# Kernel tuning notes

Measured on AMD Instinct MI355X. Metric: run time of the kernel, lower is better.

Reference implementation:

```python
import jax, jax.numpy as jnp
import numpy as np

B, L, D_PAIR, N_HEAD = 1, 320, 128, 4
EPS = 1e-5


def setup_inputs() -> dict:
    key = jax.random.key(0)
    ks = jax.random.split(key, 8)
    s = 0.05  # ~xavier scale for fan_in=128
    return {
        "pair": jax.random.normal(ks[0], (B, L, L, D_PAIR), jnp.float32),
        "norm_w": jnp.ones((D_PAIR,), jnp.float32),
        "norm_b": jnp.zeros((D_PAIR,), jnp.float32),
        "Wq": jax.random.normal(ks[1], (D_PAIR, D_PAIR), jnp.float32) * s,
        "Wk": jax.random.normal(ks[2], (D_PAIR, D_PAIR), jnp.float32) * s,
        "Wv": jax.random.normal(ks[3], (D_PAIR, D_PAIR), jnp.float32) * s,
        "Wg": jax.random.normal(ks[4], (D_PAIR, D_PAIR), jnp.float32) * s,
        "bg": jnp.zeros((D_PAIR,), jnp.float32),
        "Wo": jax.random.normal(ks[5], (D_PAIR, D_PAIR), jnp.float32) * s,
        "bo": jnp.zeros((D_PAIR,), jnp.float32),
        "Wb": jax.random.normal(ks[6], (N_HEAD, D_PAIR), jnp.float32) * s,
    }


def reference(pair, norm_w, norm_b, Wq, Wk, Wv, Wg, bg, Wo, bo, Wb):
    # Triangle attention, mode='start' (no permute). pair: (B, L, L, D)
    Bs, Ls, _, D = pair.shape
    H = Wb.shape[0]
    Dh = D // H
    scale = Dh ** -0.5

    # LayerNorm (fp32, matches torch eps=1e-5)
    mu = jnp.mean(pair, axis=-1, keepdims=True)
    var = jnp.var(pair, axis=-1, keepdims=True)
    x = (pair - mu) * jax.lax.rsqrt(var + EPS) * norm_w + norm_b

    def heads(y):
        # (B,L,L,D) -> (B,L,H,L,Dh): attention runs along the second L axis per row i
        return y.reshape(Bs, Ls, Ls, H, Dh).transpose(0, 1, 3, 2, 4)

    Q = heads(x @ Wq.T)
    K = heads(x @ Wk.T)
    V = heads(x @ Wv.T)
    g = heads(jax.nn.sigmoid(x @ Wg.T + bg))

    attn = jnp.einsum('blhid,blhjd->blhij', Q, K) * scale  # (B,L,H,L,L)
    # bias from RAW pair (pre-norm), projected to heads, broadcast over query index i
    bias = (pair @ Wb.T).transpose(0, 1, 3, 2)[:, :, :, None, :]  # (B,L,H,1,L)
    attn = jax.nn.softmax(attn + bias, axis=-1)

    out = jnp.einsum('blhij,blhjd->blhid', attn, V)  # (B,L,H,L,Dh)
    out = (g * out).transpose(0, 1, 3, 2, 4).reshape(Bs, Ls, Ls, D)
    return pair + out @ Wo.T + bo
```

## Files before the change

kernel.cpp:

```cpp
#include <hip/hip_runtime.h>

typedef unsigned short u16;
typedef unsigned int u32;
typedef __attribute__((ext_vector_type(8))) short bf16x8;
typedef __attribute__((ext_vector_type(4))) float f32x4;
typedef __attribute__((ext_vector_type(2))) unsigned int u32x2;

#define LOG2E 1.4426950408889634f

__device__ __forceinline__ u16 f2bf(float f) {
    u32 u = __float_as_uint(f);
    u += 0x7fffu + ((u >> 16) & 1u);
    return (u16)(u >> 16);
}
__device__ __forceinline__ u32 pk_bf_trunc(float hi, float lo) {
    return __builtin_amdgcn_perm(__float_as_uint(hi), __float_as_uint(lo), 0x07060302u);
}

__global__ void wconv_kernel(const float* __restrict__ Wq, const float* __restrict__ Wk,
                             const float* __restrict__ Wv, const float* __restrict__ Wg,
                             const float* __restrict__ Wo, const float* __restrict__ norm_w,
                             const float* __restrict__ norm_b, const float* __restrict__ bg,
                             u16* __restrict__ wbf, float* __restrict__ cvec) {
    int b = blockIdx.x;
    if (b < 64) {
        int idx = b * 256 + threadIdx.x;
        float w = norm_w[idx & 127];
        wbf[0 * 16384 + idx] = f2bf(Wq[idx] * w);
        wbf[1 * 16384 + idx] = f2bf(Wk[idx] * w);
        wbf[2 * 16384 + idx] = f2bf(Wv[idx] * w);
        wbf[3 * 16384 + idx] = f2bf(Wg[idx] * w);
        wbf[4 * 16384 + idx] = f2bf(Wo[idx]);
    } else {
        int m = b - 64;
        int n = threadIdx.x;
        if (n < 128) {
            const float* W = (m == 0) ? Wq : (m == 1) ? Wk : (m == 2) ? Wv : Wg;
            float c = 0.f;
#pragma unroll
            for (int k4 = 0; k4 < 32; ++k4) {
                f32x4 bb = *(const f32x4*)&norm_b[k4 * 4];
                f32x4 ww = *(const f32x4*)&W[n * 128 + k4 * 4];
                c += bb[0] * ww[0] + bb[1] * ww[1] + bb[2] * ww[2] + bb[3] * ww[3];
            }
            if (m == 3) c += bg[n];
            cvec[m * 128 + n] = c;
        }
    }
}

#define KS_OFF 9216
#define VTS_OFF 22016
#define PB_W 1152

__global__ __launch_bounds__(512, 4)
void attn_kernel(const float* __restrict__ pair,
                 const float* __restrict__ Wb,
                 const u16* __restrict__ wbf,
                 const float* __restrict__ cvec,
                 u16* __restrict__ Obf,
                 u16* __restrict__ Gg) {
    const int l = blockIdx.x >> 2;
    const int h = blockIdx.x & 3;
    const int tid = threadIdx.x;
    const int wave = tid >> 6;
    const int lane = tid & 63;
    const int i_lo = lane & 15;
    const int q = lane >> 4;

    __shared__ __align__(16) u16 smem[32576];
    __shared__ __align__(16) float biasLds[320];

    const int row_g = tid >> 3;
    const int c8 = tid & 7;
    const int wrow = (wave & 3) * 16;
    const int nth_flip = wave >> 2;

    f32x4 wbv[4];
#pragma unroll
    for (int u = 0; u < 4; ++u)
        wbv[u] = *(const f32x4*)&Wb[h * 128 + c8 * 16 + u * 4];

    float cQ[2], cK[2], cV[2], cG[2];
#pragma unroll
    for (int half = 0; half < 2; ++half) {
        int n = h * 32 + half * 16 + i_lo;
        cQ[half] = cvec[0 * 128 + n];
        cK[half] = cvec[1 * 128 + n];
        cV[half] = cvec[2 * 128 + n];
        cG[half] = cvec[3 * 128 + n];
    }

    u32 qkeep[3][4];

#pragma unroll 1
    for (int t = 0; t < 5; ++t) {
        const int j0 = t * 64;
        const float* prow = pair + ((size_t)(l * 320 + j0 + row_g)) * 128 + c8 * 16;
        f32x4 pr[4];
#pragma unroll
        for (int u = 0; u < 4; ++u) pr[u] = *(const f32x4*)(prow + u * 4);

        float s = 0.f, s2 = 0.f, bd = 0.f;
#pragma unroll
        for (int u = 0; u < 4; ++u) {
            f32x4 p = pr[u];
            f32x4 wb4 = wbv[u];
            s += p[0] + p[1] + p[2] + p[3];
            s2 += p[0] * p[0] + p[1] * p[1] + p[2] * p[2] + p[3] * p[3];
            bd += p[0] * wb4[0] + p[1] * wb4[1] + p[2] * wb4[2] + p[3] * wb4[3];
        }
        s += __shfl_xor(s, 1);   s += __shfl_xor(s, 2);   s += __shfl_xor(s, 4);
        s2 += __shfl_xor(s2, 1); s2 += __shfl_xor(s2, 2); s2 += __shfl_xor(s2, 4);
        bd += __shfl_xor(bd, 1); bd += __shfl_xor(bd, 2); bd += __shfl_xor(bd, 4);
        float mu = s * 0.0078125f;
        float var = s2 * 0.0078125f - mu * mu;
        float rs = rsqrtf(var + 1e-5f);

        __syncthreads();
#pragma unroll
        for (int u = 0; u < 4; ++u) {
            f32x4 p = pr[u];
            ushort4 xv;
            xv.x = f2bf((p[0] - mu) * rs);
            xv.y = f2bf((p[1] - mu) * rs);
            xv.z = f2bf((p[2] - mu) * rs);
            xv.w = f2bf((p[3] - mu) * rs);
            *(ushort4*)&smem[row_g * 136 + c8 * 16 + u * 4] = xv;
        }
        if (c8 == 0) biasLds[j0 + row_g] = bd * LOG2E;
        __syncthreads();

        const int nth = (t & 1) ^ nth_flip;
        f32x4 acc[4];
#pragma unroll
        for (int n2 = 0; n2 < 4; ++n2) acc[n2] = (f32x4){0.f, 0.f, 0.f, 0.f};
#pragma unroll
        for (int kc = 0; kc < 4; ++kc) {
            bf16x8 a = *(const bf16x8*)&smem[(wrow + i_lo) * 136 + kc * 32 + q * 8];
#pragma unroll
            for (int n2 = 0; n2 < 4; ++n2) {
                int nt = nth * 4 + n2;
                bf16x8 wf = *(const bf16x8*)&wbf[(nt >> 1) * 16384 +
                                                 (h * 32 + (nt & 1) * 16 + i_lo) * 128 + kc * 32 + q * 8];
                acc[n2] = __builtin_amdgcn_mfma_f32_16x16x32_bf16(a, wf, acc[n2], 0, 0, 0);
            }
        }
        const int jrow = j0 + wrow + q * 4;
        if (nth == 0) {
            const int ti = t >> 1;
#pragma unroll
            for (int dd = 0; dd < 2; ++dd)
#pragma unroll
                for (int rr = 0; rr < 2; ++rr)
                    qkeep[ti][dd * 2 + rr] =
                        (u32)f2bf(acc[dd][rr * 2] + cQ[dd]) |
                        ((u32)f2bf(acc[dd][rr * 2 + 1] + cQ[dd]) << 16);
#pragma unroll
            for (int n2 = 2; n2 < 4; ++n2)
#pragma unroll
                for (int r = 0; r < 4; ++r)
                    smem[KS_OFF + (jrow + r) * 40 + (n2 & 1) * 16 + i_lo] =
                        f2bf(acc[n2][r] + cK[n2 & 1]);
        } else {
#pragma unroll
            for (int n2 = 0; n2 < 2; ++n2)
#pragma unroll
                for (int r = 0; r < 4; ++r)
                    smem[VTS_OFF + (n2 * 16 + i_lo) * 330 + jrow + r] =
                        f2bf(acc[n2][r] + cV[n2]);
#pragma unroll
            for (int n2 = 2; n2 < 4; ++n2)
#pragma unroll
                for (int r = 0; r < 4; ++r) {
                    float z = acc[n2][r] + cG[n2 & 1];
                    float g = 1.0f / (1.0f + exp2f(-z * LOG2E));
                    Gg[((size_t)((l * 4 + h) * 320 + jrow + r)) * 32 + (n2 & 1) * 16 + i_lo] = f2bf(g);
                }
        }
    }
    __syncthreads();

    const float SC = 0.17677669529663687f * LOG2E;
    const f32x4 zero4 = {0.f, 0.f, 0.f, 0.f};
    u16* pb = smem + wave * PB_W;
    const int nstrip = (wave < 4) ? 3 : 2;
#pragma unroll 1
    for (int t2 = 0; t2 < nstrip; ++t2) {
        const int i0 = (wave + 8 * t2) * 16;
#pragma unroll
        for (int dd = 0; dd < 2; ++dd)
#pragma unroll
            for (int rr = 0; rr < 2; ++rr) {
                u32 v = qkeep[t2][dd * 2 + rr];
                pb[(q * 4 + rr * 2) * 40 + dd * 16 + i_lo] = (u16)v;
                pb[(q * 4 + rr * 2 + 1) * 40 + dd * 16 + i_lo] = (u16)(v >> 16);
            }
        bf16x8 qf = *(const bf16x8*)&pb[i_lo * 40 + q * 8];

        f32x4 oacc[2];
        oacc[0] = zero4; oacc[1] = zero4;
        float sum = 0.f;
#pragma unroll 1
        for (int c = 0; c < 5; ++c) {
            f32x4 sc4[4];
#pragma unroll
            for (int jt = 0; jt < 4; ++jt) {
                bf16x8 kf = *(const bf16x8*)&smem[KS_OFF + (c * 64 + jt * 16 + i_lo) * 40 + q * 8];
                sc4[jt] = __builtin_amdgcn_mfma_f32_16x16x32_bf16(kf, qf, zero4, 0, 0, 0);
            }
#pragma unroll
            for (int jt = 0; jt < 4; ++jt) {
                f32x4 b4 = *(const f32x4*)&biasLds[c * 64 + jt * 16 + q * 4];
#pragma unroll
                for (int r = 0; r < 4; ++r) {
                    float p = exp2f(sc4[jt][r] * SC + b4[r]);
                    sc4[jt][r] = p;
                    sum += p;
                }
            }
#pragma unroll
            for (int jt = 0; jt < 4; ++jt) {
                u32x2 pk;
                pk.x = pk_bf_trunc(sc4[jt][1], sc4[jt][0]);
                pk.y = pk_bf_trunc(sc4[jt][3], sc4[jt][2]);
                *(u32x2*)&pb[i_lo * 72 + jt * 16 + q * 4] = pk;
            }
#pragma unroll
            for (int kt2 = 0; kt2 < 2; ++kt2) {
                bf16x8 pf = *(const bf16x8*)&pb[i_lo * 72 + kt2 * 32 + q * 8];
#pragma unroll
                for (int mt = 0; mt < 2; ++mt) {
                    bf16x8 vf = *(const bf16x8*)&smem[VTS_OFF + (mt * 16 + i_lo) * 330 +
                                                      c * 64 + kt2 * 32 + q * 8];
                    oacc[mt] = __builtin_amdgcn_mfma_f32_16x16x32_bf16(vf, pf, oacc[mt], 0, 0, 0);
                }
            }
        }
        sum += __shfl_xor(sum, 16);
        sum += __shfl_xor(sum, 32);
        float rinv = 1.0f / sum;
#pragma unroll
        for (int mt = 0; mt < 2; ++mt) {
            u32x2 pk;
            pk.x = pk_bf_trunc(oacc[mt][1] * rinv, oacc[mt][0] * rinv);
            pk.y = pk_bf_trunc(oacc[mt][3] * rinv, oacc[mt][2] * rinv);
            *(u32x2*)&Obf[((size_t)(l * 320 + i0 + i_lo)) * 128 + h * 32 + mt * 16 + q * 4] = pk;
        }
    }
}

__global__ __launch_bounds__(512, 6)
void outproj_kernel(const float* __restrict__ pair,
                    const float* __restrict__ bo,
                    const u16* __restrict__ Obf,
                    const u16* __restrict__ Gg,
                    const u16* __restrict__ wbf,
                    float* __restrict__ out) {
    const int tid = threadIdx.x;
    const int wave = tid >> 6;
    const int lane = tid & 63;
    const int i_lo = lane & 15;
    const int q = lane >> 4;

    __shared__ __align__(16) u16 WoLds[128 * 132];
    const u16* Wo = wbf + 4 * 16384;
#pragma unroll
    for (int it = 0; it < 4; ++it) {
        int unit = it * 512 + tid;
        int n = unit >> 4, k8 = unit & 15;
        *(bf16x8*)&WoLds[n * 132 + k8 * 8] = *(const bf16x8*)&Wo[unit * 8];
    }
    __syncthreads();

    const int row0 = blockIdx.x * 128 + wave * 16;
    const int lidx = row0 / 320;
    const int irow = row0 - lidx * 320 + i_lo;

    bf16x8 of[4];
#pragma unroll
    for (int kc = 0; kc < 4; ++kc) {
        union { bf16x8 v; u32 u[4]; } A, G, R;
        A.v = *(const bf16x8*)&Obf[((size_t)(row0 + i_lo)) * 128 + kc * 32 + q * 8];
        G.v = *(const bf16x8*)&Gg[((size_t)((lidx * 4 + kc) * 320 + irow)) * 32 + q * 8];
#pragma unroll
        for (int k4 = 0; k4 < 4; ++k4) {
            float lo = __uint_as_float(A.u[k4] << 16) * __uint_as_float(G.u[k4] << 16);
            float hi = __uint_as_float(A.u[k4] & 0xffff0000u) * __uint_as_float(G.u[k4] & 0xffff0000u);
            R.u[k4] = pk_bf_trunc(hi, lo);
        }
        of[kc] = R.v;
    }

    f32x4 acc[8];
#pragma unroll
    for (int nt = 0; nt < 8; ++nt) acc[nt] = (f32x4){0.f, 0.f, 0.f, 0.f};
#pragma unroll
    for (int nt = 0; nt < 8; ++nt) {
#pragma unroll
        for (int kc = 0; kc < 4; ++kc) {
            bf16x8 wf = *(const bf16x8*)&WoLds[(nt * 16 + i_lo) * 132 + kc * 32 + q * 8];
            acc[nt] = __builtin_amdgcn_mfma_f32_16x16x32_bf16(wf, of[kc], acc[nt], 0, 0, 0);
        }
    }
#pragma unroll
    for (int nt = 0; nt < 8; ++nt) {
        size_t idx = ((size_t)(row0 + i_lo)) * 128 + nt * 16 + q * 4;
        f32x4 p4 = *(const f32x4*)&pair[idx];
        f32x4 b4 = *(const f32x4*)&bo[nt * 16 + q * 4];
        f32x4 o4;
        o4[0] = acc[nt][0] + p4[0] + b4[0];
        o4[1] = acc[nt][1] + p4[1] + b4[1];
        o4[2] = acc[nt][2] + p4[2] + b4[2];
        o4[3] = acc[nt][3] + p4[3] + b4[3];
        *(f32x4*)&out[idx] = o4;
    }
}

extern "C" void kernel_launch(void* const* d_in, const int* in_sizes, int n_in,
                              void* d_out, int out_size, void* d_ws, size_t ws_size,
                              hipStream_t stream) {
    const float* pair   = (const float*)d_in[0];
    const float* norm_w = (const float*)d_in[1];
    const float* norm_b = (const float*)d_in[2];
    const float* Wq     = (const float*)d_in[3];
    const float* Wk     = (const float*)d_in[4];
    const float* Wv     = (const float*)d_in[5];
    const float* Wg     = (const float*)d_in[6];
    const float* bg     = (const float*)d_in[7];
    const float* Wo     = (const float*)d_in[8];
    const float* bo     = (const float*)d_in[9];
    const float* Wb     = (const float*)d_in[10];

    u16* wbf    = (u16*)d_ws;
    float* cvec = (float*)(wbf + 5 * 16384);
    u16* Obf    = (u16*)(cvec + 512);
    u16* Gg     = Obf + (size_t)102400 * 128;
    float* out  = (float*)d_out;

    wconv_kernel<<<68, 256, 0, stream>>>(Wq, Wk, Wv, Wg, Wo, norm_w, norm_b, bg, wbf, cvec);
    attn_kernel<<<320 * 4, 512, 0, stream>>>(pair, Wb, wbf, cvec, Obf, Gg);
    outproj_kernel<<<800, 512, 0, stream>>>(pair, bo, Obf, Gg, wbf, out);
}
```

Measured before the change: 280.5 us.

## Prefetch pair rows, software-pipeline QK MFMAs, fuse gating into attention, reshape outproj

The attention kernel now loads the next 64-row pair tile right after the sync, so the global load overlaps the projection MFMAs. In the attention loop, the QK score MFMAs for the next chunk are issued before the PV MFMAs, and the PV block runs at raised wave priority. The sigmoid gate multiply moves from outproj into the attention epilogue, so outproj no longer reads Gg. Outproj switches to 256-thread blocks with an XOR-swizzled, unpadded Wo LDS layout and issues the Obf load before staging Wo. These changes cost extra registers for the prefetched tiles and the double-buffered scores, which may lower attention occupancy.

```diff
diff --git a/kernel.cpp b/kernel.cpp
--- a/kernel.cpp
+++ b/kernel.cpp
@@ -93,13 +93,14 @@
 
     u32 qkeep[3][4];
 
+    const float* prowb = pair + ((size_t)(l * 320 + row_g)) * 128 + c8 * 16;
+    f32x4 pr[4];
+#pragma unroll
+    for (int u = 0; u < 4; ++u) pr[u] = *(const f32x4*)(prowb + u * 4);
+
 #pragma unroll 1
     for (int t = 0; t < 5; ++t) {
         const int j0 = t * 64;
-        const float* prow = pair + ((size_t)(l * 320 + j0 + row_g)) * 128 + c8 * 16;
-        f32x4 pr[4];
-#pragma unroll
-        for (int u = 0; u < 4; ++u) pr[u] = *(const f32x4*)(prow + u * 4);
 
         float s = 0.f, s2 = 0.f, bd = 0.f;
 #pragma unroll
@@ -131,6 +132,12 @@
         if (c8 == 0) biasLds[j0 + row_g] = bd * LOG2E;
         __syncthreads();
 
+        if (t < 4) {
+            const float* prow = prowb + (size_t)(t + 1) * 64 * 128;
+#pragma unroll
+            for (int u = 0; u < 4; ++u) pr[u] = *(const f32x4*)(prow + u * 4);
+        }
+
         const int nth = (t & 1) ^ nth_flip;
         f32x4 acc[4];
 #pragma unroll
@@ -201,14 +208,15 @@
         f32x4 oacc[2];
         oacc[0] = zero4; oacc[1] = zero4;
         float sum = 0.f;
+
+        f32x4 sc4[4];
+#pragma unroll
+        for (int jt = 0; jt < 4; ++jt) {
+            bf16x8 kf = *(const bf16x8*)&smem[KS_OFF + (jt * 16 + i_lo) * 40 + q * 8];
+            sc4[jt] = __builtin_amdgcn_mfma_f32_16x16x32_bf16(kf, qf, zero4, 0, 0, 0);
+        }
 #pragma unroll 1
         for (int c = 0; c < 5; ++c) {
-            f32x4 sc4[4];
-#pragma unroll
-            for (int jt = 0; jt < 4; ++jt) {
-                bf16x8 kf = *(const bf16x8*)&smem[KS_OFF + (c * 64 + jt * 16 + i_lo) * 40 + q * 8];
-                sc4[jt] = __builtin_amdgcn_mfma_f32_16x16x32_bf16(kf, qf, zero4, 0, 0, 0);
-            }
 #pragma unroll
             for (int jt = 0; jt < 4; ++jt) {
                 f32x4 b4 = *(const f32x4*)&biasLds[c * 64 + jt * 16 + q * 4];
@@ -226,6 +234,15 @@
                 pk.y = pk_bf_trunc(sc4[jt][3], sc4[jt][2]);
                 *(u32x2*)&pb[i_lo * 72 + jt * 16 + q * 4] = pk;
             }
+            f32x4 sc4n[4];
+            if (c < 4) {
+#pragma unroll
+                for (int jt = 0; jt < 4; ++jt) {
+                    bf16x8 kf = *(const bf16x8*)&smem[KS_OFF + ((c + 1) * 64 + jt * 16 + i_lo) * 40 + q * 8];
+                    sc4n[jt] = __builtin_amdgcn_mfma_f32_16x16x32_bf16(kf, qf, zero4, 0, 0, 0);
+                }
+            }
+            __builtin_amdgcn_s_setprio(1);
 #pragma unroll
             for (int kt2 = 0; kt2 < 2; ++kt2) {
                 bf16x8 pf = *(const bf16x8*)&pb[i_lo * 72 + kt2 * 32 + q * 8];
@@ -236,25 +253,38 @@
                     oacc[mt] = __builtin_amdgcn_mfma_f32_16x16x32_bf16(vf, pf, oacc[mt], 0, 0, 0);
                 }
             }
-        }
+            __builtin_amdgcn_s_setprio(0);
+            if (c < 4) {
+#pragma unroll
+                for (int jt = 0; jt < 4; ++jt) sc4[jt] = sc4n[jt];
+            }
+        }
+        const size_t gbase = ((size_t)((l * 4 + h) * 320 + i0 + i_lo)) * 32;
+        u32x2 gv0 = *(const u32x2*)&Gg[gbase + 0 * 16 + q * 4];
+        u32x2 gv1 = *(const u32x2*)&Gg[gbase + 1 * 16 + q * 4];
+
         sum += __shfl_xor(sum, 16);
         sum += __shfl_xor(sum, 32);
         float rinv = 1.0f / sum;
 #pragma unroll
         for (int mt = 0; mt < 2; ++mt) {
+            u32x2 gv = mt ? gv1 : gv0;
+            float g0 = __uint_as_float(gv.x << 16);
+            float g1 = __uint_as_float(gv.x & 0xffff0000u);
+            float g2 = __uint_as_float(gv.y << 16);
+            float g3 = __uint_as_float(gv.y & 0xffff0000u);
             u32x2 pk;
-            pk.x = pk_bf_trunc(oacc[mt][1] * rinv, oacc[mt][0] * rinv);
-            pk.y = pk_bf_trunc(oacc[mt][3] * rinv, oacc[mt][2] * rinv);
+            pk.x = pk_bf_trunc(oacc[mt][1] * rinv * g1, oacc[mt][0] * rinv * g0);
+            pk.y = pk_bf_trunc(oacc[mt][3] * rinv * g3, oacc[mt][2] * rinv * g2);
             *(u32x2*)&Obf[((size_t)(l * 320 + i0 + i_lo)) * 128 + h * 32 + mt * 16 + q * 4] = pk;
         }
     }
 }
 
-__global__ __launch_bounds__(512, 6)
+__global__ __launch_bounds__(256, 4)
 void outproj_kernel(const float* __restrict__ pair,
                     const float* __restrict__ bo,
                     const u16* __restrict__ Obf,
-                    const u16* __restrict__ Gg,
                     const u16* __restrict__ wbf,
                     float* __restrict__ out) {
     const int tid = threadIdx.x;
@@ -263,35 +293,24 @@
     const int i_lo = lane & 15;
     const int q = lane >> 4;
 
-    __shared__ __align__(16) u16 WoLds[128 * 132];
+    __shared__ __align__(16) u16 WoLds[128 * 128];
+
+    const int row0 = blockIdx.x * 64 + wave * 16;
+
+    bf16x8 of[4];
+#pragma unroll
+    for (int kc = 0; kc < 4; ++kc)
+        of[kc] = *(const bf16x8*)&Obf[((size_t)(row0 + i_lo)) * 128 + kc * 32 + q * 8];
+
     const u16* Wo = wbf + 4 * 16384;
 #pragma unroll
-    for (int it = 0; it < 4; ++it) {
-        int unit = it * 512 + tid;
+    for (int it = 0; it < 8; ++it) {
+        int unit = it * 256 + tid;
         int n = unit >> 4, k8 = unit & 15;
-        *(bf16x8*)&WoLds[n * 132 + k8 * 8] = *(const bf16x8*)&Wo[unit * 8];
+        *(bf16x8*)&WoLds[n * 128 + ((k8 ^ (n & 15)) * 8)] = *(const bf16x8*)&Wo[unit * 8];
     }
     __syncthreads();
 
-    const int row0 = blockIdx.x * 128 + wave * 16;
-    const int lidx = row0 / 320;
-    const int irow = row0 - lidx * 320 + i_lo;
-
-    bf16x8 of[4];
-#pragma unroll
-    for (int kc = 0; kc < 4; ++kc) {
-        union { bf16x8 v; u32 u[4]; } A, G, R;
-        A.v = *(const bf16x8*)&Obf[((size_t)(row0 + i_lo)) * 128 + kc * 32 + q * 8];
-        G.v = *(const bf16x8*)&Gg[((size_t)((lidx * 4 + kc) * 320 + irow)) * 32 + q * 8];
-#pragma unroll
-        for (int k4 = 0; k4 < 4; ++k4) {
-            float lo = __uint_as_float(A.u[k4] << 16) * __uint_as_float(G.u[k4] << 16);
-            float hi = __uint_as_float(A.u[k4] & 0xffff0000u) * __uint_as_float(G.u[k4] & 0xffff0000u);
-            R.u[k4] = pk_bf_trunc(hi, lo);
-        }
-        of[kc] = R.v;
-    }
-
     f32x4 acc[8];
 #pragma unroll
     for (int nt = 0; nt < 8; ++nt) acc[nt] = (f32x4){0.f, 0.f, 0.f, 0.f};
@@ -299,7 +318,7 @@
     for (int nt = 0; nt < 8; ++nt) {
 #pragma unroll
         for (int kc = 0; kc < 4; ++kc) {
-            bf16x8 wf = *(const bf16x8*)&WoLds[(nt * 16 + i_lo) * 132 + kc * 32 + q * 8];
+            bf16x8 wf = *(const bf16x8*)&WoLds[(nt * 16 + i_lo) * 128 + (((kc * 4 + q) ^ i_lo) * 8)];
             acc[nt] = __builtin_amdgcn_mfma_f32_16x16x32_bf16(wf, of[kc], acc[nt], 0, 0, 0);
         }
     }
@@ -340,5 +359,5 @@
 
     wconv_kernel<<<68, 256, 0, stream>>>(Wq, Wk, Wv, Wg, Wo, norm_w, norm_b, bg, wbf, cvec);
     attn_kernel<<<320 * 4, 512, 0, stream>>>(pair, Wb, wbf, cvec, Obf, Gg);
-    outproj_kernel<<<800, 512, 0, stream>>>(pair, bo, Obf, Gg, wbf, out);
-}
+    outproj_kernel<<<1600, 256, 0, stream>>>(pair, bo, Obf, wbf, out);
+}
```

Measured after the change: 286.7 us. 2.2% more time.

## Remap attention blocks per XCD, MFMA row sums, and resize out-projection blocks

Applied to the files above, without the earlier changes.

The attention kernel now maps block IDs so that the four heads of one row l land on the same XCD, which should improve L2 reuse of that row's pair data. The softmax denominator is computed with an extra MFMA against a ones vector instead of per-lane adds and cross-lane shuffles. The out-projection kernel moves to 256-thread blocks over 64 rows, replaces padded Wo LDS rows with an XOR-swizzled layout, and issues the Obf/Gg global loads before the Wo staging so their latency overlaps. The trade-offs are one extra MFMA per chunk and Wo staged into LDS by twice as many blocks.

```diff
diff --git a/kernel.cpp b/kernel.cpp
--- a/kernel.cpp
+++ b/kernel.cpp
@@ -60,8 +60,11 @@
                  const float* __restrict__ cvec,
                  u16* __restrict__ Obf,
                  u16* __restrict__ Gg) {
-    const int l = blockIdx.x >> 2;
-    const int h = blockIdx.x & 3;
+    const int bid = blockIdx.x;
+    const int xcd = bid & 7;
+    const int s_i = bid >> 3;
+    const int h = s_i & 3;
+    const int l = ((s_i >> 2) << 3) | xcd;
     const int tid = threadIdx.x;
     const int wave = tid >> 6;
     const int lane = tid & 63;
@@ -183,6 +186,9 @@
 
     const float SC = 0.17677669529663687f * LOG2E;
     const f32x4 zero4 = {0.f, 0.f, 0.f, 0.f};
+    union { bf16x8 v; u32 u[4]; } onesf;
+#pragma unroll
+    for (int u = 0; u < 4; ++u) onesf.u[u] = 0x3F803F80u;
     u16* pb = smem + wave * PB_W;
     const int nstrip = (wave < 4) ? 3 : 2;
 #pragma unroll 1
@@ -200,7 +206,7 @@
 
         f32x4 oacc[2];
         oacc[0] = zero4; oacc[1] = zero4;
-        float sum = 0.f;
+        f32x4 sacc = zero4;
 #pragma unroll 1
         for (int c = 0; c < 5; ++c) {
             f32x4 sc4[4];
@@ -213,11 +219,8 @@
             for (int jt = 0; jt < 4; ++jt) {
                 f32x4 b4 = *(const f32x4*)&biasLds[c * 64 + jt * 16 + q * 4];
 #pragma unroll
-                for (int r = 0; r < 4; ++r) {
-                    float p = exp2f(sc4[jt][r] * SC + b4[r]);
-                    sc4[jt][r] = p;
-                    sum += p;
-                }
+                for (int r = 0; r < 4; ++r)
+                    sc4[jt][r] = exp2f(sc4[jt][r] * SC + b4[r]);
             }
 #pragma unroll
             for (int jt = 0; jt < 4; ++jt) {
@@ -229,6 +232,7 @@
 #pragma unroll
             for (int kt2 = 0; kt2 < 2; ++kt2) {
                 bf16x8 pf = *(const bf16x8*)&pb[i_lo * 72 + kt2 * 32 + q * 8];
+                sacc = __builtin_amdgcn_mfma_f32_16x16x32_bf16(onesf.v, pf, sacc, 0, 0, 0);
 #pragma unroll
                 for (int mt = 0; mt < 2; ++mt) {
                     bf16x8 vf = *(const bf16x8*)&smem[VTS_OFF + (mt * 16 + i_lo) * 330 +
@@ -237,9 +241,7 @@
                 }
             }
         }
-        sum += __shfl_xor(sum, 16);
-        sum += __shfl_xor(sum, 32);
-        float rinv = 1.0f / sum;
+        float rinv = 1.0f / sacc[0];
 #pragma unroll
         for (int mt = 0; mt < 2; ++mt) {
             u32x2 pk;
@@ -250,7 +252,7 @@
     }
 }
 
-__global__ __launch_bounds__(512, 6)
+__global__ __launch_bounds__(256, 4)
 void outproj_kernel(const float* __restrict__ pair,
                     const float* __restrict__ bo,
                     const u16* __restrict__ Obf,
@@ -263,30 +265,36 @@
     const int i_lo = lane & 15;
     const int q = lane >> 4;
 
-    __shared__ __align__(16) u16 WoLds[128 * 132];
-    const u16* Wo = wbf + 4 * 16384;
-#pragma unroll
-    for (int it = 0; it < 4; ++it) {
-        int unit = it * 512 + tid;
-        int n = unit >> 4, k8 = unit & 15;
-        *(bf16x8*)&WoLds[n * 132 + k8 * 8] = *(const bf16x8*)&Wo[unit * 8];
-    }
-    __syncthreads();
-
-    const int row0 = blockIdx.x * 128 + wave * 16;
+    __shared__ __align__(16) u16 WoLds[128 * 128];
+
+    const int row0 = blockIdx.x * 64 + wave * 16;
     const int lidx = row0 / 320;
     const int irow = row0 - lidx * 320 + i_lo;
 
+    union { bf16x8 v; u32 u[4]; } A[4], G[4];
+#pragma unroll
+    for (int kc = 0; kc < 4; ++kc) {
+        A[kc].v = *(const bf16x8*)&Obf[((size_t)(row0 + i_lo)) * 128 + kc * 32 + q * 8];
+        G[kc].v = *(const bf16x8*)&Gg[((size_t)((lidx * 4 + kc) * 320 + irow)) * 32 + q * 8];
+    }
+
+    const u16* Wo = wbf + 4 * 16384;
+#pragma unroll
+    for (int it = 0; it < 8; ++it) {
+        int unit = it * 256 + tid;
+        int n = unit >> 4, k8 = unit & 15;
+        *(bf16x8*)&WoLds[n * 128 + ((k8 ^ (n & 15)) * 8)] = *(const bf16x8*)&Wo[unit * 8];
+    }
+    __syncthreads();
+
     bf16x8 of[4];
 #pragma unroll
     for (int kc = 0; kc < 4; ++kc) {
-        union { bf16x8 v; u32 u[4]; } A, G, R;
-        A.v = *(const bf16x8*)&Obf[((size_t)(row0 + i_lo)) * 128 + kc * 32 + q * 8];
-        G.v = *(const bf16x8*)&Gg[((size_t)((lidx * 4 + kc) * 320 + irow)) * 32 + q * 8];
+        union { bf16x8 v; u32 u[4]; } R;
 #pragma unroll
         for (int k4 = 0; k4 < 4; ++k4) {
-            float lo = __uint_as_float(A.u[k4] << 16) * __uint_as_float(G.u[k4] << 16);
-            float hi = __uint_as_float(A.u[k4] & 0xffff0000u) * __uint_as_float(G.u[k4] & 0xffff0000u);
+            float lo = __uint_as_float(A[kc].u[k4] << 16) * __uint_as_float(G[kc].u[k4] << 16);
+            float hi = __uint_as_float(A[kc].u[k4] & 0xffff0000u) * __uint_as_float(G[kc].u[k4] & 0xffff0000u);
             R.u[k4] = pk_bf_trunc(hi, lo);
         }
         of[kc] = R.v;
@@ -299,7 +307,7 @@
     for (int nt = 0; nt < 8; ++nt) {
 #pragma unroll
         for (int kc = 0; kc < 4; ++kc) {
-            bf16x8 wf = *(const bf16x8*)&WoLds[(nt * 16 + i_lo) * 132 + kc * 32 + q * 8];
+            bf16x8 wf = *(const bf16x8*)&WoLds[(nt * 16 + i_lo) * 128 + (((kc * 4 + q) ^ i_lo) * 8)];
             acc[nt] = __builtin_amdgcn_mfma_f32_16x16x32_bf16(wf, of[kc], acc[nt], 0, 0, 0);
         }
     }
@@ -340,5 +348,5 @@
 
     wconv_kernel<<<68, 256, 0, stream>>>(Wq, Wk, Wv, Wg, Wo, norm_w, norm_b, bg, wbf, cvec);
     attn_kernel<<<320 * 4, 512, 0, stream>>>(pair, Wb, wbf, cvec, Obf, Gg);
-    outproj_kernel<<<800, 512, 0, stream>>>(pair, bo, Obf, Gg, wbf, out);
-}
+    outproj_kernel<<<1600, 256, 0, stream>>>(pair, bo, Obf, Gg, wbf, out);
+}
```

Result: no change. 279.4 us (median of 2 runs) (-0.4%).
